# Kernel optimization log

Measured on AMD Instinct MI355X. Metric: run time of the kernel, lower is better.

## Reference

```python
import jax, jax.numpy as jnp
import numpy as np

DIM = 768
N_HEADS = 12
HEAD_DIM = DIM // N_HEADS
B, T = 2, 2048


def setup_inputs() -> dict:
    key = jax.random.key(0)
    ks = jax.random.split(key, 11)
    s = 0.02
    return {
        "q_in": jax.random.normal(ks[0], (B, T, DIM), jnp.float32),
        "k_in": jax.random.normal(ks[1], (B, T, DIM), jnp.float32),
        "v_in": jax.random.normal(ks[2], (B, T, DIM), jnp.float32),
        "Wq": jax.random.normal(ks[3], (DIM, DIM), jnp.float32) * s,
        "bq": jnp.zeros((DIM,), jnp.float32),
        "Wk": jax.random.normal(ks[4], (DIM, DIM), jnp.float32) * s,
        "bk": jnp.zeros((DIM,), jnp.float32),
        "Wv": jax.random.normal(ks[5], (DIM, DIM), jnp.float32) * s,
        "bv": jnp.zeros((DIM,), jnp.float32),
        "Wo": jax.random.normal(ks[6], (DIM, DIM), jnp.float32) * s,
        "bo": jnp.zeros((DIM,), jnp.float32),
    }


def reference(q_in, k_in, v_in, Wq, bq, Wk, bk, Wv, bv, Wo, bo):
    b, t, c = q_in.shape
    scale = HEAD_DIM ** -0.5
    # linear projections (torch Linear: x @ W.T + b)
    q = q_in @ Wq.T + bq
    k = k_in @ Wk.T + bk
    v = v_in @ Wv.T + bv
    # [b, t, h, d] -> [b, h, t, d]
    q = q.reshape(b, t, N_HEADS, HEAD_DIM).transpose(0, 2, 1, 3)
    k = k.reshape(b, t, N_HEADS, HEAD_DIM).transpose(0, 2, 1, 3)
    v = v.reshape(b, t, N_HEADS, HEAD_DIM).transpose(0, 2, 1, 3)
    scores = jnp.einsum("bhqd,bhkd->bhqk", q, k) * scale  # full TxT scores
    probs = jax.nn.softmax(scores, axis=-1)
    attn = jnp.einsum("bhqk,bhkd->bhqd", probs, v)
    attn = attn.transpose(0, 2, 1, 3).reshape(b, t, c)
    return attn @ Wo.T + bo
```

## Files before the change

kernel.cpp:

```cpp
#include <hip/hip_runtime.h>


typedef unsigned short u16;
typedef __attribute__((ext_vector_type(8))) short short8;
typedef __attribute__((ext_vector_type(4))) float float4v;

#define DIMC 768
#define NTOK 4096
#define NHD  12
#define HDD  64
#define SEQT 2048

__device__ __forceinline__ u16 f2bf(float f) {
  union { float f; unsigned u; } v; v.f = f;
  unsigned r = v.u + 0x7fffu + ((v.u >> 16) & 1u);
  return (u16)(r >> 16);
}
__device__ __forceinline__ float bf2f(u16 u) {
  union { unsigned u; float f; } v; v.u = ((unsigned)u) << 16;
  return v.f;
}

__global__ __launch_bounds__(256) void cvt3_kernel(
    const float* __restrict__ a, const float* __restrict__ b, const float* __restrict__ c,
    u16* __restrict__ oa, u16* __restrict__ ob, u16* __restrict__ oc) {
  int z = blockIdx.y;
  const float* s = (z == 0) ? a : (z == 1) ? b : c;
  u16* d = (z == 0) ? oa : (z == 1) ? ob : oc;
  size_t i = ((size_t)blockIdx.x * 256 + threadIdx.x) * 4;
  float4 v = *(const float4*)(s + i);
  *(ushort4*)(d + i) = make_ushort4(f2bf(v.x), f2bf(v.y), f2bf(v.z), f2bf(v.w));
}

__global__ __launch_bounds__(256) void cvt4_kernel(
    const float* __restrict__ a, const float* __restrict__ b,
    const float* __restrict__ c, const float* __restrict__ e,
    u16* __restrict__ oa, u16* __restrict__ ob, u16* __restrict__ oc, u16* __restrict__ oe) {
  int z = blockIdx.y;
  const float* s = (z == 0) ? a : (z == 1) ? b : (z == 2) ? c : e;
  u16* d = (z == 0) ? oa : (z == 1) ? ob : (z == 2) ? oc : oe;
  size_t i = ((size_t)blockIdx.x * 256 + threadIdx.x) * 4;
  float4 v = *(const float4*)(s + i);
  *(ushort4*)(d + i) = make_ushort4(f2bf(v.x), f2bf(v.y), f2bf(v.z), f2bf(v.w));
}

__device__ __forceinline__ void gemm_mainloop2(
    const u16* __restrict__ X, const u16* __restrict__ W,
    int m0, int n0, u16* Als, u16* Bls, float4v acc[4][2]) {
  int tid = threadIdx.x;
  int sr = tid >> 3, sc = (tid & 7) * 8;
  int w = tid >> 6, lane = tid & 63, quad = lane >> 4, r15 = lane & 15;
  int wm = (w >> 1) * 64, wn = (w & 1) * 32;
  const u16* xp0 = X + (size_t)(m0 + sr) * DIMC + sc;
  const u16* xp1 = xp0 + 32 * DIMC;
  const u16* xp2 = xp0 + 64 * DIMC;
  const u16* xp3 = xp0 + 96 * DIMC;
  const u16* wp0 = W + (size_t)(n0 + sr) * DIMC + sc;
  const u16* wp1 = wp0 + 32 * DIMC;
  uint4 pa0 = *(const uint4*)xp0, pa1 = *(const uint4*)xp1;
  uint4 pa2 = *(const uint4*)xp2, pa3 = *(const uint4*)xp3;
  uint4 pb0 = *(const uint4*)wp0, pb1 = *(const uint4*)wp1;
  for (int k0 = 0; k0 < DIMC; k0 += 64) {
    __syncthreads();
    *(uint4*)(Als + sr * 72 + sc) = pa0;
    *(uint4*)(Als + (sr + 32) * 72 + sc) = pa1;
    *(uint4*)(Als + (sr + 64) * 72 + sc) = pa2;
    *(uint4*)(Als + (sr + 96) * 72 + sc) = pa3;
    *(uint4*)(Bls + sr * 72 + sc) = pb0;
    *(uint4*)(Bls + (sr + 32) * 72 + sc) = pb1;
    __syncthreads();
    int kn = k0 + 64;
    if (kn < DIMC) {
      pa0 = *(const uint4*)(xp0 + kn); pa1 = *(const uint4*)(xp1 + kn);
      pa2 = *(const uint4*)(xp2 + kn); pa3 = *(const uint4*)(xp3 + kn);
      pb0 = *(const uint4*)(wp0 + kn); pb1 = *(const uint4*)(wp1 + kn);
    }
    #pragma unroll
    for (int sk = 0; sk < 2; sk++) {
      short8 af[4], bf[2];
      #pragma unroll
      for (int mf = 0; mf < 4; mf++)
        af[mf] = *(const short8*)(Als + (wm + mf * 16 + r15) * 72 + sk * 32 + quad * 8);
      #pragma unroll
      for (int nf = 0; nf < 2; nf++)
        bf[nf] = *(const short8*)(Bls + (wn + nf * 16 + r15) * 72 + sk * 32 + quad * 8);
      #pragma unroll
      for (int mf = 0; mf < 4; mf++)
        #pragma unroll
        for (int nf = 0; nf < 2; nf++)
          acc[mf][nf] = __builtin_amdgcn_mfma_f32_16x16x32_bf16(af[mf], bf[nf], acc[mf][nf], 0, 0, 0);
    }
  }
}

__global__ __launch_bounds__(256, 4) void gemm_qkv(
    const u16* __restrict__ xq, const u16* __restrict__ xk, const u16* __restrict__ xv,
    const u16* __restrict__ wq, const u16* __restrict__ wk, const u16* __restrict__ wv,
    const float* __restrict__ bq, const float* __restrict__ bk, const float* __restrict__ bv,
    u16* __restrict__ Qh, u16* __restrict__ Kh, u16* __restrict__ Vt) {
  __shared__ __align__(16) u16 Als[128 * 72];
  __shared__ __align__(16) u16 Bls[64 * 72];
  int z = blockIdx.z;
  const u16* X = (z == 0) ? xq : (z == 1) ? xk : xv;
  const u16* W = (z == 0) ? wq : (z == 1) ? wk : wv;
  const float* bias = (z == 0) ? bq : (z == 1) ? bk : bv;
  int m0 = blockIdx.x * 128, n0 = blockIdx.y * 64;
  float4v acc[4][2];
  #pragma unroll
  for (int i = 0; i < 4; i++)
    #pragma unroll
    for (int j = 0; j < 2; j++)
      #pragma unroll
      for (int r = 0; r < 4; r++) acc[i][j][r] = 0.f;
  gemm_mainloop2(X, W, m0, n0, Als, Bls, acc);
  int tid = threadIdx.x, w = tid >> 6, lane = tid & 63, quad = lane >> 4, r15 = lane & 15;
  int wm = (w >> 1) * 64, wn = (w & 1) * 32;
  #pragma unroll
  for (int mf = 0; mf < 4; mf++)
    #pragma unroll
    for (int nf = 0; nf < 2; nf++)
      #pragma unroll
      for (int rg = 0; rg < 4; rg++) {
        int m = m0 + wm + mf * 16 + quad * 4 + rg;
        int n = n0 + wn + nf * 16 + r15;
        float val = acc[mf][nf][rg] + bias[n];
        int b = m >> 11, t = m & 2047, h = n >> 6, d = n & 63;
        u16 o = f2bf(val);
        size_t bh = (size_t)(b * NHD + h);
        if (z == 2) Vt[(bh * HDD + d) * SEQT + t] = o;
        else if (z == 0) Qh[(bh * SEQT + t) * HDD + d] = o;
        else Kh[(bh * SEQT + t) * HDD + d] = o;
      }
}

__global__ __launch_bounds__(256, 3) void attn_kernel(
    const u16* __restrict__ Qh, const u16* __restrict__ Kh, const u16* __restrict__ Vt,
    u16* __restrict__ Opart, float* __restrict__ Lpart) {
  constexpr float CEXP = 0.125f * 1.44269504088896f;
  __shared__ __align__(16) u16 Kls[64 * 72];
  __shared__ __align__(16) u16 Vls[64 * 72];
  __shared__ __align__(16) u16 Pls[4 * 32 * 72];
  int bh = blockIdx.y, kv = blockIdx.z, qt0 = blockIdx.x * 128;
  int tid = threadIdx.x, w = tid >> 6, lane = tid & 63, quad = lane >> 4, r15 = lane & 15;
  int qw = qt0 + w * 32;

  short8 qa[2][2];
  #pragma unroll
  for (int qs = 0; qs < 2; qs++) {
    const u16* qp = Qh + ((size_t)bh * SEQT + qw + qs * 16 + r15) * HDD + quad * 8;
    qa[qs][0] = *(const short8*)qp;
    qa[qs][1] = *(const short8*)(qp + 32);
  }
  short8 ones;
  #pragma unroll
  for (int i = 0; i < 8; i++) ones[i] = (short)0x3F80;

  float4v oacc[2][4], lacc[2];
  #pragma unroll
  for (int qs = 0; qs < 2; qs++) {
    #pragma unroll
    for (int r = 0; r < 4; r++) lacc[qs][r] = 0.f;
    #pragma unroll
    for (int dt = 0; dt < 4; dt++)
      #pragma unroll
      for (int r = 0; r < 4; r++) oacc[qs][dt][r] = 0.f;
  }

  const u16* Kbase = Kh + (size_t)bh * SEQT * HDD;
  const u16* Vbase = Vt + (size_t)bh * HDD * SEQT;
  u16* Pw = Pls + w * (32 * 72);
  int sr = tid >> 3, sc = (tid & 7) * 8;
  int kt0 = kv * 1024;

  uint4 pk0 = *(const uint4*)(Kbase + (size_t)(kt0 + sr) * HDD + sc);
  uint4 pk1 = *(const uint4*)(Kbase + (size_t)(kt0 + sr + 32) * HDD + sc);
  uint4 pv0 = *(const uint4*)(Vbase + (size_t)sr * SEQT + kt0 + sc);
  uint4 pv1 = *(const uint4*)(Vbase + (size_t)(sr + 32) * SEQT + kt0 + sc);

  for (int it = 0; it < 16; it++) {
    __syncthreads();
    *(uint4*)(Kls + sr * 72 + sc) = pk0;
    *(uint4*)(Kls + (sr + 32) * 72 + sc) = pk1;
    *(uint4*)(Vls + sr * 72 + sc) = pv0;
    *(uint4*)(Vls + (sr + 32) * 72 + sc) = pv1;
    __syncthreads();
    int ktn = kt0 + ((it + 1) & 15) * 64;
    pk0 = *(const uint4*)(Kbase + (size_t)(ktn + sr) * HDD + sc);
    pk1 = *(const uint4*)(Kbase + (size_t)(ktn + sr + 32) * HDD + sc);
    pv0 = *(const uint4*)(Vbase + (size_t)sr * SEQT + ktn + sc);
    pv1 = *(const uint4*)(Vbase + (size_t)(sr + 32) * SEQT + ktn + sc);

    float4v st[4][2];
    #pragma unroll
    for (int nk = 0; nk < 4; nk++) {
      short8 k0 = *(const short8*)(Kls + (nk * 16 + r15) * 72 + quad * 8);
      short8 k1 = *(const short8*)(Kls + (nk * 16 + r15) * 72 + 32 + quad * 8);
      #pragma unroll
      for (int qs = 0; qs < 2; qs++) {
        float4v z;
        #pragma unroll
        for (int r = 0; r < 4; r++) z[r] = 0.f;
        z = __builtin_amdgcn_mfma_f32_16x16x32_bf16(k0, qa[qs][0], z, 0, 0, 0);
        z = __builtin_amdgcn_mfma_f32_16x16x32_bf16(k1, qa[qs][1], z, 0, 0, 0);
        st[nk][qs] = z;
      }
    }
    #pragma unroll
    for (int qs = 0; qs < 2; qs++)
      #pragma unroll
      for (int nk = 0; nk < 4; nk++) {
        float p0 = exp2f(st[nk][qs][0] * CEXP);
        float p1 = exp2f(st[nk][qs][1] * CEXP);
        float p2 = exp2f(st[nk][qs][2] * CEXP);
        float p3 = exp2f(st[nk][qs][3] * CEXP);
        unsigned lo = __builtin_amdgcn_perm(__float_as_uint(p1), __float_as_uint(p0), 0x07060302u);
        unsigned hi = __builtin_amdgcn_perm(__float_as_uint(p3), __float_as_uint(p2), 0x07060302u);
        *(uint2*)(Pw + (qs * 16 + r15) * 72 + nk * 16 + quad * 4) = make_uint2(lo, hi);
      }
    short8 pa[2][2];
    #pragma unroll
    for (int qs = 0; qs < 2; qs++) {
      pa[qs][0] = *(const short8*)(Pw + (qs * 16 + r15) * 72 + quad * 8);
      pa[qs][1] = *(const short8*)(Pw + (qs * 16 + r15) * 72 + 32 + quad * 8);
      lacc[qs] = __builtin_amdgcn_mfma_f32_16x16x32_bf16(pa[qs][0], ones, lacc[qs], 0, 0, 0);
      lacc[qs] = __builtin_amdgcn_mfma_f32_16x16x32_bf16(pa[qs][1], ones, lacc[qs], 0, 0, 0);
    }
    #pragma unroll
    for (int dt = 0; dt < 4; dt++) {
      short8 v0 = *(const short8*)(Vls + (dt * 16 + r15) * 72 + quad * 8);
      short8 v1 = *(const short8*)(Vls + (dt * 16 + r15) * 72 + 32 + quad * 8);
      #pragma unroll
      for (int qs = 0; qs < 2; qs++) {
        oacc[qs][dt] = __builtin_amdgcn_mfma_f32_16x16x32_bf16(pa[qs][0], v0, oacc[qs][dt], 0, 0, 0);
        oacc[qs][dt] = __builtin_amdgcn_mfma_f32_16x16x32_bf16(pa[qs][1], v1, oacc[qs][dt], 0, 0, 0);
      }
    }
  }
  size_t obase = ((size_t)kv * 2 * NHD + bh) * SEQT;
  #pragma unroll
  for (int qs = 0; qs < 2; qs++)
    #pragma unroll
    for (int rg = 0; rg < 4; rg++) {
      int q = qw + qs * 16 + quad * 4 + rg;
      u16* orow = Opart + (obase + q) * HDD;
      #pragma unroll
      for (int dt = 0; dt < 4; dt++) orow[dt * 16 + r15] = f2bf(oacc[qs][dt][rg]);
      if (r15 == 0) Lpart[obase + q] = lacc[qs][rg];
    }
}

__global__ __launch_bounds__(256) void merge_kernel(
    const u16* __restrict__ Opart, const float* __restrict__ Lpart, u16* __restrict__ X2) {
  int tid = threadIdx.x;
  int row = blockIdx.x * 32 + (tid >> 3);
  int dcol = (tid & 7) * 8;
  int bh = row >> 11, t = row & 2047;
  size_t off1 = (size_t)row * HDD + dcol;
  size_t off2 = off1 + (size_t)2 * NHD * SEQT * HDD;
  ushort4 a0 = *(const ushort4*)(Opart + off1);
  ushort4 a1 = *(const ushort4*)(Opart + off1 + 4);
  ushort4 b0 = *(const ushort4*)(Opart + off2);
  ushort4 b1 = *(const ushort4*)(Opart + off2 + 4);
  float inv = 1.0f / (Lpart[row] + Lpart[row + 2 * NHD * SEQT]);
  int b = bh / NHD, h = bh % NHD;
  u16 o[8];
  o[0] = f2bf((bf2f(a0.x) + bf2f(b0.x)) * inv);
  o[1] = f2bf((bf2f(a0.y) + bf2f(b0.y)) * inv);
  o[2] = f2bf((bf2f(a0.z) + bf2f(b0.z)) * inv);
  o[3] = f2bf((bf2f(a0.w) + bf2f(b0.w)) * inv);
  o[4] = f2bf((bf2f(a1.x) + bf2f(b1.x)) * inv);
  o[5] = f2bf((bf2f(a1.y) + bf2f(b1.y)) * inv);
  o[6] = f2bf((bf2f(a1.z) + bf2f(b1.z)) * inv);
  o[7] = f2bf((bf2f(a1.w) + bf2f(b1.w)) * inv);
  *(uint4*)(X2 + ((size_t)b * SEQT + t) * DIMC + h * HDD + dcol) = *(uint4*)o;
}

__global__ __launch_bounds__(256, 4) void gemm_out(
    const u16* __restrict__ X2, const u16* __restrict__ wo,
    const float* __restrict__ bo, float* __restrict__ out) {
  __shared__ __align__(16) u16 Als[128 * 72];
  __shared__ __align__(16) u16 Bls[64 * 72];
  int m0 = blockIdx.x * 128, n0 = blockIdx.y * 64;
  float4v acc[4][2];
  #pragma unroll
  for (int i = 0; i < 4; i++)
    #pragma unroll
    for (int j = 0; j < 2; j++)
      #pragma unroll
      for (int r = 0; r < 4; r++) acc[i][j][r] = 0.f;
  gemm_mainloop2(X2, wo, m0, n0, Als, Bls, acc);
  int tid = threadIdx.x, w = tid >> 6, lane = tid & 63, quad = lane >> 4, r15 = lane & 15;
  int wm = (w >> 1) * 64, wn = (w & 1) * 32;
  #pragma unroll
  for (int mf = 0; mf < 4; mf++)
    #pragma unroll
    for (int nf = 0; nf < 2; nf++)
      #pragma unroll
      for (int rg = 0; rg < 4; rg++) {
        int m = m0 + wm + mf * 16 + quad * 4 + rg;
        int n = n0 + wn + nf * 16 + r15;
        out[(size_t)m * DIMC + n] = acc[mf][nf][rg] + bo[n];
      }
}

extern "C" void kernel_launch(void* const* d_in, const int* in_sizes, int n_in,
                              void* d_out, int out_size, void* d_ws, size_t ws_size,
                              hipStream_t stream) {
  const float* q_in = (const float*)d_in[0];
  const float* k_in = (const float*)d_in[1];
  const float* v_in = (const float*)d_in[2];
  const float* Wq = (const float*)d_in[3];
  const float* bq = (const float*)d_in[4];
  const float* Wk = (const float*)d_in[5];
  const float* bk = (const float*)d_in[6];
  const float* Wv = (const float*)d_in[7];
  const float* bv = (const float*)d_in[8];
  const float* Wo = (const float*)d_in[9];
  const float* bo = (const float*)d_in[10];

  const size_t NX = (size_t)NTOK * DIMC;
  const size_t NW = (size_t)DIMC * DIMC;
  u16* ws = (u16*)d_ws;
  u16* qb = ws;
  u16* kb = qb + NX;
  u16* vb = kb + NX;
  u16* wqb = vb + NX;
  u16* wkb = wqb + NW;
  u16* wvb = wkb + NW;
  u16* wob = wvb + NW;
  u16* Qh = wob + NW;
  u16* Kh = Qh + NX;
  u16* Vt = Kh + NX;
  u16* X2 = Vt + NX;
  u16* Opart = qb;
  float* Lpart = (float*)(ws + 2 * NX);

  cvt3_kernel<<<dim3(NX / 1024, 3), 256, 0, stream>>>(q_in, k_in, v_in, qb, kb, vb);
  cvt4_kernel<<<dim3(NW / 1024, 4), 256, 0, stream>>>(Wq, Wk, Wv, Wo, wqb, wkb, wvb, wob);
  gemm_qkv<<<dim3(NTOK / 128, DIMC / 64, 3), 256, 0, stream>>>(
      qb, kb, vb, wqb, wkb, wvb, bq, bk, bv, Qh, Kh, Vt);
  attn_kernel<<<dim3(SEQT / 128, 2 * NHD, 2), 256, 0, stream>>>(Qh, Kh, Vt, Opart, Lpart);
  merge_kernel<<<dim3(2 * NHD * SEQT / 32), 256, 0, stream>>>(Opart, Lpart, X2);
  gemm_out<<<dim3(NTOK / 128, DIMC / 64), 256, 0, stream>>>(X2, wob, bo, (float*)d_out);
}
```

Before: 199.9 us.

## Merge convert kernels, retile QKV and output GEMMs, fold softmax scale into Q

Merges the two fp32-to-bf16 conversion kernels into one launch, with early exit for the smaller weight tensors. The QKV GEMM tile grows to 128x128 for more reuse per block, while the output GEMM shrinks to 64x64 tiles so more blocks can fill the device. The softmax scale times log2(e) is folded into Q in the projection epilogue, which removes a multiply per score in attention. Attention prefetch now uses incrementing pointers and skips the wasted last load, and the launch-bounds occupancy hints are dropped, which may change register allocation and occupancy.

Measured after the change: 281.8 us. 41.0% more time.

```diff
diff --git a/kernel.cpp b/kernel.cpp
--- a/kernel.cpp
+++ b/kernel.cpp
@@ -10,6 +10,7 @@
 #define NHD  12
 #define HDD  64
 #define SEQT 2048
+#define CEXPQ 0.1803368757f
 
 __device__ __forceinline__ u16 f2bf(float f) {
   union { float f; unsigned u; } v; v.f = f;
@@ -21,109 +22,104 @@
   return v.f;
 }
 
-__global__ __launch_bounds__(256) void cvt3_kernel(
-    const float* __restrict__ a, const float* __restrict__ b, const float* __restrict__ c,
-    u16* __restrict__ oa, u16* __restrict__ ob, u16* __restrict__ oc) {
+__global__ __launch_bounds__(256) void cvt_all(
+    const float* __restrict__ i0, const float* __restrict__ i1, const float* __restrict__ i2,
+    const float* __restrict__ w0, const float* __restrict__ w1,
+    const float* __restrict__ w2, const float* __restrict__ w3,
+    u16* __restrict__ o0, u16* __restrict__ o1, u16* __restrict__ o2,
+    u16* __restrict__ p0, u16* __restrict__ p1, u16* __restrict__ p2, u16* __restrict__ p3) {
   int z = blockIdx.y;
-  const float* s = (z == 0) ? a : (z == 1) ? b : c;
-  u16* d = (z == 0) ? oa : (z == 1) ? ob : oc;
+  const float* s; u16* d; size_t lim;
+  switch (z) {
+    case 0: s = i0; d = o0; lim = (size_t)NTOK * DIMC; break;
+    case 1: s = i1; d = o1; lim = (size_t)NTOK * DIMC; break;
+    case 2: s = i2; d = o2; lim = (size_t)NTOK * DIMC; break;
+    case 3: s = w0; d = p0; lim = (size_t)DIMC * DIMC; break;
+    case 4: s = w1; d = p1; lim = (size_t)DIMC * DIMC; break;
+    case 5: s = w2; d = p2; lim = (size_t)DIMC * DIMC; break;
+    default: s = w3; d = p3; lim = (size_t)DIMC * DIMC; break;
+  }
   size_t i = ((size_t)blockIdx.x * 256 + threadIdx.x) * 4;
+  if (i >= lim) return;
   float4 v = *(const float4*)(s + i);
   *(ushort4*)(d + i) = make_ushort4(f2bf(v.x), f2bf(v.y), f2bf(v.z), f2bf(v.w));
 }
 
-__global__ __launch_bounds__(256) void cvt4_kernel(
-    const float* __restrict__ a, const float* __restrict__ b,
-    const float* __restrict__ c, const float* __restrict__ e,
-    u16* __restrict__ oa, u16* __restrict__ ob, u16* __restrict__ oc, u16* __restrict__ oe) {
-  int z = blockIdx.y;
-  const float* s = (z == 0) ? a : (z == 1) ? b : (z == 2) ? c : e;
-  u16* d = (z == 0) ? oa : (z == 1) ? ob : (z == 2) ? oc : oe;
-  size_t i = ((size_t)blockIdx.x * 256 + threadIdx.x) * 4;
-  float4 v = *(const float4*)(s + i);
-  *(ushort4*)(d + i) = make_ushort4(f2bf(v.x), f2bf(v.y), f2bf(v.z), f2bf(v.w));
-}
-
-__device__ __forceinline__ void gemm_mainloop2(
-    const u16* __restrict__ X, const u16* __restrict__ W,
-    int m0, int n0, u16* Als, u16* Bls, float4v acc[4][2]) {
-  int tid = threadIdx.x;
-  int sr = tid >> 3, sc = (tid & 7) * 8;
-  int w = tid >> 6, lane = tid & 63, quad = lane >> 4, r15 = lane & 15;
-  int wm = (w >> 1) * 64, wn = (w & 1) * 32;
-  const u16* xp0 = X + (size_t)(m0 + sr) * DIMC + sc;
-  const u16* xp1 = xp0 + 32 * DIMC;
-  const u16* xp2 = xp0 + 64 * DIMC;
-  const u16* xp3 = xp0 + 96 * DIMC;
-  const u16* wp0 = W + (size_t)(n0 + sr) * DIMC + sc;
-  const u16* wp1 = wp0 + 32 * DIMC;
-  uint4 pa0 = *(const uint4*)xp0, pa1 = *(const uint4*)xp1;
-  uint4 pa2 = *(const uint4*)xp2, pa3 = *(const uint4*)xp3;
-  uint4 pb0 = *(const uint4*)wp0, pb1 = *(const uint4*)wp1;
-  for (int k0 = 0; k0 < DIMC; k0 += 64) {
-    __syncthreads();
-    *(uint4*)(Als + sr * 72 + sc) = pa0;
-    *(uint4*)(Als + (sr + 32) * 72 + sc) = pa1;
-    *(uint4*)(Als + (sr + 64) * 72 + sc) = pa2;
-    *(uint4*)(Als + (sr + 96) * 72 + sc) = pa3;
-    *(uint4*)(Bls + sr * 72 + sc) = pb0;
-    *(uint4*)(Bls + (sr + 32) * 72 + sc) = pb1;
-    __syncthreads();
-    int kn = k0 + 64;
-    if (kn < DIMC) {
-      pa0 = *(const uint4*)(xp0 + kn); pa1 = *(const uint4*)(xp1 + kn);
-      pa2 = *(const uint4*)(xp2 + kn); pa3 = *(const uint4*)(xp3 + kn);
-      pb0 = *(const uint4*)(wp0 + kn); pb1 = *(const uint4*)(wp1 + kn);
-    }
-    #pragma unroll
-    for (int sk = 0; sk < 2; sk++) {
-      short8 af[4], bf[2];
-      #pragma unroll
-      for (int mf = 0; mf < 4; mf++)
-        af[mf] = *(const short8*)(Als + (wm + mf * 16 + r15) * 72 + sk * 32 + quad * 8);
-      #pragma unroll
-      for (int nf = 0; nf < 2; nf++)
-        bf[nf] = *(const short8*)(Bls + (wn + nf * 16 + r15) * 72 + sk * 32 + quad * 8);
-      #pragma unroll
-      for (int mf = 0; mf < 4; mf++)
-        #pragma unroll
-        for (int nf = 0; nf < 2; nf++)
-          acc[mf][nf] = __builtin_amdgcn_mfma_f32_16x16x32_bf16(af[mf], bf[nf], acc[mf][nf], 0, 0, 0);
-    }
-  }
-}
-
-__global__ __launch_bounds__(256, 4) void gemm_qkv(
+__global__ __launch_bounds__(256) void gemm_qkv(
     const u16* __restrict__ xq, const u16* __restrict__ xk, const u16* __restrict__ xv,
     const u16* __restrict__ wq, const u16* __restrict__ wk, const u16* __restrict__ wv,
     const float* __restrict__ bq, const float* __restrict__ bk, const float* __restrict__ bv,
     u16* __restrict__ Qh, u16* __restrict__ Kh, u16* __restrict__ Vt) {
   __shared__ __align__(16) u16 Als[128 * 72];
-  __shared__ __align__(16) u16 Bls[64 * 72];
+  __shared__ __align__(16) u16 Bls[128 * 72];
   int z = blockIdx.z;
   const u16* X = (z == 0) ? xq : (z == 1) ? xk : xv;
   const u16* W = (z == 0) ? wq : (z == 1) ? wk : wv;
   const float* bias = (z == 0) ? bq : (z == 1) ? bk : bv;
-  int m0 = blockIdx.x * 128, n0 = blockIdx.y * 64;
-  float4v acc[4][2];
+  int m0 = blockIdx.x * 128, n0 = blockIdx.y * 128;
+  int tid = threadIdx.x;
+  int sr = tid >> 3, sc = (tid & 7) * 8;
+  int w = tid >> 6, lane = tid & 63, quad = lane >> 4, r15 = lane & 15;
+  int wm = (w >> 1) * 64, wn = (w & 1) * 64;
+
+  float4v acc[4][4];
   #pragma unroll
   for (int i = 0; i < 4; i++)
     #pragma unroll
-    for (int j = 0; j < 2; j++)
+    for (int j = 0; j < 4; j++)
       #pragma unroll
       for (int r = 0; r < 4; r++) acc[i][j][r] = 0.f;
-  gemm_mainloop2(X, W, m0, n0, Als, Bls, acc);
-  int tid = threadIdx.x, w = tid >> 6, lane = tid & 63, quad = lane >> 4, r15 = lane & 15;
-  int wm = (w >> 1) * 64, wn = (w & 1) * 32;
+
+  const u16* xp = X + (size_t)(m0 + sr) * DIMC + sc;
+  const u16* wp = W + (size_t)(n0 + sr) * DIMC + sc;
+  uint4 pa[4], pb[4];
+  #pragma unroll
+  for (int r = 0; r < 4; r++) {
+    pa[r] = *(const uint4*)(xp + r * 32 * DIMC);
+    pb[r] = *(const uint4*)(wp + r * 32 * DIMC);
+  }
+  for (int k0 = 0; k0 < DIMC; k0 += 64) {
+    __syncthreads();
+    #pragma unroll
+    for (int r = 0; r < 4; r++) {
+      *(uint4*)(Als + (sr + r * 32) * 72 + sc) = pa[r];
+      *(uint4*)(Bls + (sr + r * 32) * 72 + sc) = pb[r];
+    }
+    __syncthreads();
+    if (k0 + 64 < DIMC) {
+      xp += 64; wp += 64;
+      #pragma unroll
+      for (int r = 0; r < 4; r++) {
+        pa[r] = *(const uint4*)(xp + r * 32 * DIMC);
+        pb[r] = *(const uint4*)(wp + r * 32 * DIMC);
+      }
+    }
+    #pragma unroll
+    for (int sk = 0; sk < 2; sk++) {
+      short8 af[4], bf[4];
+      #pragma unroll
+      for (int mf = 0; mf < 4; mf++)
+        af[mf] = *(const short8*)(Als + (wm + mf * 16 + r15) * 72 + sk * 32 + quad * 8);
+      #pragma unroll
+      for (int nf = 0; nf < 4; nf++)
+        bf[nf] = *(const short8*)(Bls + (wn + nf * 16 + r15) * 72 + sk * 32 + quad * 8);
+      #pragma unroll
+      for (int mf = 0; mf < 4; mf++)
+        #pragma unroll
+        for (int nf = 0; nf < 4; nf++)
+          acc[mf][nf] = __builtin_amdgcn_mfma_f32_16x16x32_bf16(af[mf], bf[nf], acc[mf][nf], 0, 0, 0);
+    }
+  }
   #pragma unroll
   for (int mf = 0; mf < 4; mf++)
     #pragma unroll
-    for (int nf = 0; nf < 2; nf++)
+    for (int nf = 0; nf < 4; nf++)
       #pragma unroll
       for (int rg = 0; rg < 4; rg++) {
         int m = m0 + wm + mf * 16 + quad * 4 + rg;
         int n = n0 + wn + nf * 16 + r15;
         float val = acc[mf][nf][rg] + bias[n];
+        if (z == 0) val *= CEXPQ;
         int b = m >> 11, t = m & 2047, h = n >> 6, d = n & 63;
         u16 o = f2bf(val);
         size_t bh = (size_t)(b * NHD + h);
@@ -133,10 +129,9 @@
       }
 }
 
-__global__ __launch_bounds__(256, 3) void attn_kernel(
+__global__ __launch_bounds__(256) void attn_kernel(
     const u16* __restrict__ Qh, const u16* __restrict__ Kh, const u16* __restrict__ Vt,
     u16* __restrict__ Opart, float* __restrict__ Lpart) {
-  constexpr float CEXP = 0.125f * 1.44269504088896f;
   __shared__ __align__(16) u16 Kls[64 * 72];
   __shared__ __align__(16) u16 Vls[64 * 72];
   __shared__ __align__(16) u16 Pls[4 * 32 * 72];
@@ -166,16 +161,16 @@
       for (int r = 0; r < 4; r++) oacc[qs][dt][r] = 0.f;
   }
 
-  const u16* Kbase = Kh + (size_t)bh * SEQT * HDD;
-  const u16* Vbase = Vt + (size_t)bh * HDD * SEQT;
   u16* Pw = Pls + w * (32 * 72);
   int sr = tid >> 3, sc = (tid & 7) * 8;
   int kt0 = kv * 1024;
-
-  uint4 pk0 = *(const uint4*)(Kbase + (size_t)(kt0 + sr) * HDD + sc);
-  uint4 pk1 = *(const uint4*)(Kbase + (size_t)(kt0 + sr + 32) * HDD + sc);
-  uint4 pv0 = *(const uint4*)(Vbase + (size_t)sr * SEQT + kt0 + sc);
-  uint4 pv1 = *(const uint4*)(Vbase + (size_t)(sr + 32) * SEQT + kt0 + sc);
+  const u16* pK0 = Kh + (size_t)bh * SEQT * HDD + (size_t)(kt0 + sr) * HDD + sc;
+  const u16* pK1 = pK0 + 32 * HDD;
+  const u16* pV0 = Vt + (size_t)bh * HDD * SEQT + (size_t)sr * SEQT + kt0 + sc;
+  const u16* pV1 = pV0 + 32 * SEQT;
+
+  uint4 pk0 = *(const uint4*)pK0, pk1 = *(const uint4*)pK1;
+  uint4 pv0 = *(const uint4*)pV0, pv1 = *(const uint4*)pV1;
 
   for (int it = 0; it < 16; it++) {
     __syncthreads();
@@ -184,11 +179,11 @@
     *(uint4*)(Vls + sr * 72 + sc) = pv0;
     *(uint4*)(Vls + (sr + 32) * 72 + sc) = pv1;
     __syncthreads();
-    int ktn = kt0 + ((it + 1) & 15) * 64;
-    pk0 = *(const uint4*)(Kbase + (size_t)(ktn + sr) * HDD + sc);
-    pk1 = *(const uint4*)(Kbase + (size_t)(ktn + sr + 32) * HDD + sc);
-    pv0 = *(const uint4*)(Vbase + (size_t)sr * SEQT + ktn + sc);
-    pv1 = *(const uint4*)(Vbase + (size_t)(sr + 32) * SEQT + ktn + sc);
+    if (it < 15) {
+      pK0 += 64 * HDD; pK1 += 64 * HDD; pV0 += 64; pV1 += 64;
+      pk0 = *(const uint4*)pK0; pk1 = *(const uint4*)pK1;
+      pv0 = *(const uint4*)pV0; pv1 = *(const uint4*)pV1;
+    }
 
     float4v st[4][2];
     #pragma unroll
@@ -209,10 +204,10 @@
     for (int qs = 0; qs < 2; qs++)
       #pragma unroll
       for (int nk = 0; nk < 4; nk++) {
-        float p0 = exp2f(st[nk][qs][0] * CEXP);
-        float p1 = exp2f(st[nk][qs][1] * CEXP);
-        float p2 = exp2f(st[nk][qs][2] * CEXP);
-        float p3 = exp2f(st[nk][qs][3] * CEXP);
+        float p0 = exp2f(st[nk][qs][0]);
+        float p1 = exp2f(st[nk][qs][1]);
+        float p2 = exp2f(st[nk][qs][2]);
+        float p3 = exp2f(st[nk][qs][3]);
         unsigned lo = __builtin_amdgcn_perm(__float_as_uint(p1), __float_as_uint(p0), 0x07060302u);
         unsigned hi = __builtin_amdgcn_perm(__float_as_uint(p3), __float_as_uint(p2), 0x07060302u);
         *(uint2*)(Pw + (qs * 16 + r15) * 72 + nk * 16 + quad * 4) = make_uint2(lo, hi);
@@ -275,24 +270,59 @@
   *(uint4*)(X2 + ((size_t)b * SEQT + t) * DIMC + h * HDD + dcol) = *(uint4*)o;
 }
 
-__global__ __launch_bounds__(256, 4) void gemm_out(
+__global__ __launch_bounds__(256) void gemm_out(
     const u16* __restrict__ X2, const u16* __restrict__ wo,
     const float* __restrict__ bo, float* __restrict__ out) {
-  __shared__ __align__(16) u16 Als[128 * 72];
+  __shared__ __align__(16) u16 Als[64 * 72];
   __shared__ __align__(16) u16 Bls[64 * 72];
-  int m0 = blockIdx.x * 128, n0 = blockIdx.y * 64;
-  float4v acc[4][2];
-  #pragma unroll
-  for (int i = 0; i < 4; i++)
+  int m0 = blockIdx.x * 64, n0 = blockIdx.y * 64;
+  int tid = threadIdx.x;
+  int sr = tid >> 3, sc = (tid & 7) * 8;
+  int w = tid >> 6, lane = tid & 63, quad = lane >> 4, r15 = lane & 15;
+  int wm = (w >> 1) * 32, wn = (w & 1) * 32;
+
+  float4v acc[2][2];
+  #pragma unroll
+  for (int i = 0; i < 2; i++)
     #pragma unroll
     for (int j = 0; j < 2; j++)
       #pragma unroll
       for (int r = 0; r < 4; r++) acc[i][j][r] = 0.f;
-  gemm_mainloop2(X2, wo, m0, n0, Als, Bls, acc);
-  int tid = threadIdx.x, w = tid >> 6, lane = tid & 63, quad = lane >> 4, r15 = lane & 15;
-  int wm = (w >> 1) * 64, wn = (w & 1) * 32;
-  #pragma unroll
-  for (int mf = 0; mf < 4; mf++)
+
+  const u16* xp = X2 + (size_t)(m0 + sr) * DIMC + sc;
+  const u16* wp = wo + (size_t)(n0 + sr) * DIMC + sc;
+  uint4 pa0 = *(const uint4*)xp, pa1 = *(const uint4*)(xp + 32 * DIMC);
+  uint4 pb0 = *(const uint4*)wp, pb1 = *(const uint4*)(wp + 32 * DIMC);
+  for (int k0 = 0; k0 < DIMC; k0 += 64) {
+    __syncthreads();
+    *(uint4*)(Als + sr * 72 + sc) = pa0;
+    *(uint4*)(Als + (sr + 32) * 72 + sc) = pa1;
+    *(uint4*)(Bls + sr * 72 + sc) = pb0;
+    *(uint4*)(Bls + (sr + 32) * 72 + sc) = pb1;
+    __syncthreads();
+    if (k0 + 64 < DIMC) {
+      xp += 64; wp += 64;
+      pa0 = *(const uint4*)xp; pa1 = *(const uint4*)(xp + 32 * DIMC);
+      pb0 = *(const uint4*)wp; pb1 = *(const uint4*)(wp + 32 * DIMC);
+    }
+    #pragma unroll
+    for (int sk = 0; sk < 2; sk++) {
+      short8 af[2], bf[2];
+      #pragma unroll
+      for (int mf = 0; mf < 2; mf++)
+        af[mf] = *(const short8*)(Als + (wm + mf * 16 + r15) * 72 + sk * 32 + quad * 8);
+      #pragma unroll
+      for (int nf = 0; nf < 2; nf++)
+        bf[nf] = *(const short8*)(Bls + (wn + nf * 16 + r15) * 72 + sk * 32 + quad * 8);
+      #pragma unroll
+      for (int mf = 0; mf < 2; mf++)
+        #pragma unroll
+        for (int nf = 0; nf < 2; nf++)
+          acc[mf][nf] = __builtin_amdgcn_mfma_f32_16x16x32_bf16(af[mf], bf[nf], acc[mf][nf], 0, 0, 0);
+    }
+  }
+  #pragma unroll
+  for (int mf = 0; mf < 2; mf++)
     #pragma unroll
     for (int nf = 0; nf < 2; nf++)
       #pragma unroll
@@ -335,11 +365,11 @@
   u16* Opart = qb;
   float* Lpart = (float*)(ws + 2 * NX);
 
-  cvt3_kernel<<<dim3(NX / 1024, 3), 256, 0, stream>>>(q_in, k_in, v_in, qb, kb, vb);
-  cvt4_kernel<<<dim3(NW / 1024, 4), 256, 0, stream>>>(Wq, Wk, Wv, Wo, wqb, wkb, wvb, wob);
-  gemm_qkv<<<dim3(NTOK / 128, DIMC / 64, 3), 256, 0, stream>>>(
+  cvt_all<<<dim3(NX / 1024, 7), 256, 0, stream>>>(
+      q_in, k_in, v_in, Wq, Wk, Wv, Wo, qb, kb, vb, wqb, wkb, wvb, wob);
+  gemm_qkv<<<dim3(NTOK / 128, DIMC / 128, 3), 256, 0, stream>>>(
       qb, kb, vb, wqb, wkb, wvb, bq, bk, bv, Qh, Kh, Vt);
   attn_kernel<<<dim3(SEQT / 128, 2 * NHD, 2), 256, 0, stream>>>(Qh, Kh, Vt, Opart, Lpart);
   merge_kernel<<<dim3(2 * NHD * SEQT / 32), 256, 0, stream>>>(Opart, Lpart, X2);
-  gemm_out<<<dim3(NTOK / 128, DIMC / 64), 256, 0, stream>>>(X2, wob, bo, (float*)d_out);
-}
+  gemm_out<<<dim3(NTOK / 64, DIMC / 64), 256, 0, stream>>>(X2, wob, bo, (float*)d_out);
+}
```
